# Optimization experiments

Hardware: AMD Instinct MI355X
Metric: run time of the kernel (lower is better)

## Reference

```python
import jax, jax.numpy as jnp
from jax import lax
import numpy as np

B, S = 128, 512
TARGET_SIZE = 32
T = TARGET_SIZE + 4  # tag_size, START = T-2, END = T-1


def setup_inputs() -> dict:
    key = jax.random.key(0)
    k1, k2, k3, k4 = jax.random.split(key, 4)
    feats = jax.random.normal(k1, (B, S, T), dtype=jnp.float32)
    # contiguous-prefix mask (lengths in [S//2, S])
    lengths = jax.random.randint(k2, (B,), S // 2, S + 1)
    mask = (jnp.arange(S)[None, :] < lengths[:, None]).astype(jnp.int32)
    tags = jax.random.randint(k3, (B, S), 0, TARGET_SIZE).astype(jnp.int32)
    # learned transitions, with the hard constraints from __init__
    transitions = 0.1 * jax.random.normal(k4, (T, T), dtype=jnp.float32)
    transitions = transitions.at[:, T - 2].set(-1000.0)  # nothing -> START
    transitions = transitions.at[T - 1, :].set(-1000.0)  # END -> nothing
    return {"feats": feats, "transitions": transitions, "mask": mask, "tags": tags}


def _nll(feats, transitions, mask, tags):
    # feats: (B,S,T), transitions: (T,T) with [i,j] = score(prev=i -> cur=j)
    b, s, t = feats.shape
    START, END = t - 2, t - 1
    fdtype = feats.dtype

    feats_t = jnp.swapaxes(feats, 0, 1)   # (S,B,T)
    mask_t = jnp.swapaxes(mask, 0, 1)     # (S,B)

    # ---- forward algorithm (partition function) ----
    # scores[t,b,i,j] = feats[b,t,j] + transitions[i,j]
    part0 = feats_t[0] + transitions[START][None, :]  # (B,T): alpha after step 0

    def step(part, xs):
        f_step, m_step = xs  # (B,T), (B,)
        # cur[b,i,j] = feats[b,j] + trans[i,j] + part[b,i]
        cur = f_step[:, None, :] + transitions[None, :, :] + part[:, :, None]
        new_part = jax.nn.logsumexp(cur, axis=1)  # (B,T)
        part = jnp.where(m_step[:, None].astype(bool), new_part, part)
        return part, None

    part, _ = lax.scan(step, part0, (feats_t[1:], mask_t[1:]))
    final = jax.nn.logsumexp(part[:, :, None] + transitions[None, :, :], axis=1)  # (B,T)
    forward_score = jnp.sum(final[:, END])

    # ---- gold score ----
    tags_i = tags.astype(jnp.int32)
    prev_tags = jnp.concatenate(
        [jnp.full((b, 1), START, dtype=jnp.int32), tags_i[:, :-1]], axis=1)  # (B,S)
    emit = jnp.take_along_axis(feats, tags_i[:, :, None], axis=2)[:, :, 0]    # (B,S)
    trans_sc = transitions[prev_tags, tags_i]                                  # (B,S)
    tg_energy = jnp.sum((emit + trans_sc) * mask.astype(fdtype))
    lengths = jnp.sum(mask, axis=1).astype(jnp.int32)                          # (B,)
    end_ids = jnp.take_along_axis(tags_i, (lengths - 1)[:, None], axis=1)[:, 0]
    end_energy = jnp.sum(transitions[end_ids, END])
    gold_score = tg_energy + end_energy

    # average_batch = True
    return (forward_score - gold_score) / jnp.asarray(b, fdtype)


def reference(feats, transitions, mask, tags):
    return _nll(feats, transitions, mask, tags)
```

## Files before the change

kernel.cpp:

```cpp
#include <hip/hip_runtime.h>
#include <hip/hip_bf16.h>


namespace {
constexpr int kB = 128;
constexpr int kS = 512;
constexpr int kT = 36;
constexpr int kStart = 34;
constexpr int kEnd = 35;
constexpr int kP = 16;
constexpr int kL = 32;
constexpr int kEStr = 48;

typedef __bf16 bf16x4 __attribute__((ext_vector_type(4)));
typedef short short4 __attribute__((ext_vector_type(4)));
typedef float f32x4 __attribute__((ext_vector_type(4)));

__device__ __forceinline__ float readlane_f(float v, int lane) {
    return __builtin_bit_cast(float, __builtin_amdgcn_readlane(__builtin_bit_cast(int, v), lane));
}

__device__ __forceinline__ float wave_sum(float v) {
#pragma unroll
    for (int off = 32; off; off >>= 1) v += __shfl_xor(v, off, 64);
    return v;
}

__device__ __forceinline__ int wave_sum_i(int v) {
#pragma unroll
    for (int off = 32; off; off >>= 1) v += __shfl_xor(v, off, 64);
    return v;
}

#define MF16(a, b, c) __builtin_amdgcn_mfma_f32_16x16x16bf16_1k((a), (b), (c), 0, 0, 0)


__global__ __attribute__((amdgpu_flat_work_group_size(64, 64),
                          amdgpu_waves_per_eu(2, 4)))
void crf_chunk_kernel(const float* __restrict__ feats,
                      const float* __restrict__ trans,
                      const int* __restrict__ mask,
                      __bf16* __restrict__ Hws,
                      float* __restrict__ lscws) {
    const int b = blockIdx.x;
    const int p = blockIdx.y;
    const int tid = threadIdx.x;
    const int ln = tid & 15;
    const int quad = tid >> 4;

    __shared__ __align__(16) float Etab[kL * kEStr];

    const int* mb = mask + b * kS;
    int len = 0;
    for (int k = tid; k < kS; k += 64) len += mb[k];
    len = wave_sum_i(len);

    __bf16* Hout = Hws + (size_t)(b * kP + p) * (kT * kT);
    const int cs = (p == 0) ? 1 : p * kL;
    const int ce = min((p + 1) * kL, len);
    const int nsteps = ce - cs;

    if (nsteps <= 0) {
        for (int idx = tid; idx < kT * kT; idx += 64)
            Hout[idx] = (__bf16)((idx / kT == idx % kT) ? 1.f : 0.f);
        if (tid == 0) lscws[b * kP + p] = 0.f;
        return;
    }

    const float* fb = feats + ((size_t)b * kS + cs) * kT;
    for (int idx = tid; idx < kL * kEStr; idx += 64) {
        const int tl = idx / kEStr, jj = idx % kEStr;
        Etab[idx] = (jj < kT) ? __expf(fb[tl * kT + jj]) : 1.0f;
    }
    __builtin_amdgcn_s_waitcnt(0);

    auto afrag = [&](int rt, int kc) {
        bf16x4 r;
        const int m = rt * 16 + ln;
#pragma unroll
        for (int e = 0; e < 4; ++e) {
            const int k = kc * 16 + quad * 4 + e;
            float v = 0.f;
            if (m < kT && k < kT) v = __expf(trans[k * kT + m]);
            r[e] = (__bf16)v;
        }
        return __builtin_bit_cast(short4, r);
    };
    const short4 a00 = afrag(0, 0), a01 = afrag(0, 1), a02 = afrag(0, 2);
    const short4 a10 = afrag(1, 0), a11 = afrag(1, 1), a12 = afrag(1, 2);
    const short4 a20 = afrag(2, 0), a21 = afrag(2, 1), a22 = afrag(2, 2);

    auto binit = [&](int kc, int ct) {
        bf16x4 r;
        const int n = ct * 16 + ln;
#pragma unroll
        for (int e = 0; e < 4; ++e) {
            const int k = kc * 16 + quad * 4 + e;
            r[e] = (__bf16)((k == n && k < kT) ? 1.f : 0.f);
        }
        return __builtin_bit_cast(short4, r);
    };
    short4 b00 = binit(0, 0), b01 = binit(0, 1), b02 = binit(0, 2);
    short4 b10 = binit(1, 0), b11 = binit(1, 1), b12 = binit(1, 2);
    short4 b20 = binit(2, 0), b21 = binit(2, 1), b22 = binit(2, 2);

    float logC = 0.f;
    const f32x4 z = {0.f, 0.f, 0.f, 0.f};
    for (int tl = 0; tl < nsteps; ++tl) {
        const f32x4 e0 = *(const f32x4*)&Etab[tl * kEStr + 0 + quad * 4];
        const f32x4 e1 = *(const f32x4*)&Etab[tl * kEStr + 16 + quad * 4];
        const f32x4 e2 = *(const f32x4*)&Etab[tl * kEStr + 32 + quad * 4];

        f32x4 c00 = MF16(a00, b00, z); f32x4 c01 = MF16(a00, b01, z); f32x4 c02 = MF16(a00, b02, z);
        c00 = MF16(a01, b10, c00);     c01 = MF16(a01, b11, c01);     c02 = MF16(a01, b12, c02);
        c00 = MF16(a02, b20, c00);     c01 = MF16(a02, b21, c01);     c02 = MF16(a02, b22, c02);
        f32x4 c10 = MF16(a10, b00, z); f32x4 c11 = MF16(a10, b01, z); f32x4 c12 = MF16(a10, b02, z);
        c10 = MF16(a11, b10, c10);     c11 = MF16(a11, b11, c11);     c12 = MF16(a11, b12, c12);
        c10 = MF16(a12, b20, c10);     c11 = MF16(a12, b21, c11);     c12 = MF16(a12, b22, c12);
        f32x4 c20 = MF16(a20, b00, z); f32x4 c21 = MF16(a20, b01, z); f32x4 c22 = MF16(a20, b02, z);
        c20 = MF16(a21, b10, c20);     c21 = MF16(a21, b11, c21);     c22 = MF16(a21, b12, c22);
        c20 = MF16(a22, b20, c20);     c21 = MF16(a22, b21, c21);     c22 = MF16(a22, b22, c22);

        float rs = 1.f;
        if ((tl & 3) == 3) {
            const float s = readlane_f(c00[1], 1);
            rs = __builtin_amdgcn_rcpf(s);
            logC += __logf(s);
        }
        const f32x4 s0 = e0 * rs, s1 = e1 * rs, s2 = e2 * rs;

#define PK(cv, sv) ({ const f32x4 t_ = (cv) * (sv); bf16x4 h_;                  \
        h_[0] = (__bf16)t_[0]; h_[1] = (__bf16)t_[1];                           \
        h_[2] = (__bf16)t_[2]; h_[3] = (__bf16)t_[3];                           \
        __builtin_bit_cast(short4, h_); })
        b00 = PK(c00, s0); b01 = PK(c01, s0); b02 = PK(c02, s0);
        b10 = PK(c10, s1); b11 = PK(c11, s1); b12 = PK(c12, s1);
        b20 = PK(c20, s2); b21 = PK(c21, s2); b22 = PK(c22, s2);
#undef PK
    }

#define STOREB(Bv, kc, ct) {                                                    \
    const bf16x4 h_ = __builtin_bit_cast(bf16x4, Bv);                           \
    const int n_ = (ct)*16 + ln;                                                \
    _Pragma("unroll") for (int e = 0; e < 4; ++e) {                             \
        const int m_ = (kc)*16 + quad * 4 + e;                                  \
        if (m_ < kT && n_ < kT) Hout[m_ * kT + n_] = h_[e]; } }
    STOREB(b00, 0, 0) STOREB(b01, 0, 1) STOREB(b02, 0, 2)
    STOREB(b10, 1, 0) STOREB(b11, 1, 1) STOREB(b12, 1, 2)
    STOREB(b20, 2, 0) STOREB(b21, 2, 1) STOREB(b22, 2, 2)
#undef STOREB
    if (tid == 0) lscws[b * kP + p] = logC;
}


#define FORK36(X) \
    X(0,0,0,0) X(1,1,0,1) X(2,2,0,2) X(3,3,0,3) \
    X(4,0,1,0) X(5,1,1,1) X(6,2,1,2) X(7,3,1,3) \
    X(8,0,2,0) X(9,1,2,1) X(10,2,2,2) X(11,3,2,3) \
    X(12,0,3,0) X(13,1,3,1) X(14,2,3,2) X(15,3,3,3) \
    X(16,0,4,0) X(17,1,4,1) X(18,2,4,2) X(19,3,4,3) \
    X(20,0,5,0) X(21,1,5,1) X(22,2,5,2) X(23,3,5,3) \
    X(24,0,6,0) X(25,1,6,1) X(26,2,6,2) X(27,3,6,3) \
    X(28,0,7,0) X(29,1,7,1) X(30,2,7,2) X(31,3,7,3) \
    X(32,0,8,0) X(33,1,8,1) X(34,2,8,2) X(35,3,8,3)

__global__ __attribute__((amdgpu_flat_work_group_size(64, 64),
                          amdgpu_waves_per_eu(1, 1)))
void crf_combine_kernel(const float* __restrict__ feats,
                        const float* __restrict__ trans,
                        const int* __restrict__ mask,
                        const int* __restrict__ tags,
                        const __bf16* __restrict__ Hws,
                        const float* __restrict__ lscws,
                        float* __restrict__ out) {
    const int b = blockIdx.x;
    const int j = threadIdx.x;
    const float* fbase = feats + (size_t)b * kS * kT;
    const int* mb = mask + b * kS;
    const int* tb = tags + b * kS;

    int len = 0;
    for (int k = j; k < kS; k += 64) len += mb[k];
    len = wave_sum_i(len);

    const float ME = (j < kT) ? __expf(trans[j * kT + kEnd]) : 0.f;

    float a0 = -1e30f;
    if (j < kT) a0 = fbase[j] + trans[kStart * kT + j];
    float C = readlane_f(a0, 0);
    float q = __expf(a0 - C);

    const int jr = (j < kT) ? j : 0;
#pragma unroll
    for (int p = 0; p < kP; ++p) {
        const __bf16* rp = Hws + ((size_t)(b * kP + p) * kT + jr) * kT;
        const bf16x4 h0 = *(const bf16x4*)(rp + 0);
        const bf16x4 h1 = *(const bf16x4*)(rp + 4);
        const bf16x4 h2 = *(const bf16x4*)(rp + 8);
        const bf16x4 h3 = *(const bf16x4*)(rp + 12);
        const bf16x4 h4 = *(const bf16x4*)(rp + 16);
        const bf16x4 h5 = *(const bf16x4*)(rp + 20);
        const bf16x4 h6 = *(const bf16x4*)(rp + 24);
        const bf16x4 h7 = *(const bf16x4*)(rp + 28);
        const bf16x4 h8 = *(const bf16x4*)(rp + 32);
#define BRD2(n, a, g, c) const float bb##n = readlane_f(q, n);
        FORK36(BRD2)
#undef BRD2
        float v0 = 0.f, v1 = 0.f, v2 = 0.f, v3 = 0.f;
#define FMA2(n, a, g, c) v##a = fmaf(bb##n, (float)h##g[c], v##a);
        FORK36(FMA2)
#undef FMA2
        const float qn = (v0 + v1) + (v2 + v3);
        q = (j < kT) ? qn : 0.f;
        C += lscws[b * kP + p];
        const float s = readlane_f(q, 0);
        q *= __builtin_amdgcn_rcpf(s);
        C += __logf(s);
    }

    const float ssum = wave_sum(q * ME);
    const float forward_b = C + __logf(ssum);

    float g = 0.f;
    for (int k = j; k < kS; k += 64) {
        if (k < len) {
            const int tg = tb[k];
            const int pv = (k == 0) ? kStart : tb[k - 1];
            g += fbase[(size_t)k * kT + tg] + trans[pv * kT + tg];
        }
    }
    g = wave_sum(g);

    if (j == 0) {
        g += trans[tb[len - 1] * kT + kEnd];
        atomicAdd(out, (forward_b - g) * (1.0f / kB));
    }
}

}

extern "C" void kernel_launch(void* const* d_in, const int* in_sizes, int n_in,
                              void* d_out, int out_size, void* d_ws, size_t ws_size,
                              hipStream_t stream) {
    const float* feats = (const float*)d_in[0];
    const float* trans = (const float*)d_in[1];
    const int* mask = (const int*)d_in[2];
    const int* tags = (const int*)d_in[3];
    float* out = (float*)d_out;

    __bf16* Hws = (__bf16*)d_ws;
    float* lscws = (float*)(Hws + (size_t)kB * kP * kT * kT);

    (void)hipMemsetAsync(out, 0, sizeof(float), stream);
    crf_chunk_kernel<<<dim3(kB, kP), dim3(64), 0, stream>>>(feats, trans, mask, Hws, lscws);
    crf_combine_kernel<<<dim3(kB), dim3(64), 0, stream>>>(feats, trans, mask, tags,
                                                          Hws, lscws, out);
}
```

Before: 111.4 us.

## Halve chunk length to double chunk parallelism and read rescale from bf16 state

Splits the sequence into 32 chunks of 16 steps instead of 16 chunks of 32, so each chunk kernel has a shorter serial matrix-product chain and twice as many blocks run in parallel. The combine kernel then processes twice as many chunk matrices, and its loop is only partially unrolled. The rescale factor is now read from the packed bf16 state before the MFMAs, which takes the readlane off the critical path. Feature staging and the mask sum are unrolled to batch global loads before the exp writes to LDS.

```diff
diff --git a/kernel.cpp b/kernel.cpp
--- a/kernel.cpp
+++ b/kernel.cpp
@@ -8,13 +8,14 @@
 constexpr int kT = 36;
 constexpr int kStart = 34;
 constexpr int kEnd = 35;
-constexpr int kP = 16;
-constexpr int kL = 32;
-constexpr int kEStr = 48;
+constexpr int kP = 32;
+constexpr int kL = 16;
+constexpr int kEStr = 64;
 
 typedef __bf16 bf16x4 __attribute__((ext_vector_type(4)));
-typedef short short4 __attribute__((ext_vector_type(4)));
+typedef short short4v __attribute__((ext_vector_type(4)));
 typedef float f32x4 __attribute__((ext_vector_type(4)));
+typedef int int2v __attribute__((ext_vector_type(2)));
 
 __device__ __forceinline__ float readlane_f(float v, int lane) {
     return __builtin_bit_cast(float, __builtin_amdgcn_readlane(__builtin_bit_cast(int, v), lane));
@@ -52,7 +53,8 @@
 
     const int* mb = mask + b * kS;
     int len = 0;
-    for (int k = tid; k < kS; k += 64) len += mb[k];
+#pragma unroll
+    for (int k = 0; k < kS / 64; ++k) len += mb[k * 64 + tid];
     len = wave_sum_i(len);
 
     __bf16* Hout = Hws + (size_t)(b * kP + p) * (kT * kT);
@@ -68,9 +70,14 @@
     }
 
     const float* fb = feats + ((size_t)b * kS + cs) * kT;
-    for (int idx = tid; idx < kL * kEStr; idx += 64) {
-        const int tl = idx / kEStr, jj = idx % kEStr;
-        Etab[idx] = (jj < kT) ? __expf(fb[tl * kT + jj]) : 1.0f;
+    {
+        float stage[kL];
+#pragma unroll
+        for (int it = 0; it < kL; ++it)
+            stage[it] = (tid < kT) ? fb[it * kT + tid] : 0.f;
+#pragma unroll
+        for (int it = 0; it < kL; ++it)
+            Etab[it * kEStr + tid] = (tid < kT) ? __expf(stage[it]) : 1.0f;
     }
     __builtin_amdgcn_s_waitcnt(0);
 
@@ -84,11 +91,11 @@
             if (m < kT && k < kT) v = __expf(trans[k * kT + m]);
             r[e] = (__bf16)v;
         }
-        return __builtin_bit_cast(short4, r);
+        return __builtin_bit_cast(short4v, r);
     };
-    const short4 a00 = afrag(0, 0), a01 = afrag(0, 1), a02 = afrag(0, 2);
-    const short4 a10 = afrag(1, 0), a11 = afrag(1, 1), a12 = afrag(1, 2);
-    const short4 a20 = afrag(2, 0), a21 = afrag(2, 1), a22 = afrag(2, 2);
+    const short4v a00 = afrag(0, 0), a01 = afrag(0, 1), a02 = afrag(0, 2);
+    const short4v a10 = afrag(1, 0), a11 = afrag(1, 1), a12 = afrag(1, 2);
+    const short4v a20 = afrag(2, 0), a21 = afrag(2, 1), a22 = afrag(2, 2);
 
     auto binit = [&](int kc, int ct) {
         bf16x4 r;
@@ -98,18 +105,20 @@
             const int k = kc * 16 + quad * 4 + e;
             r[e] = (__bf16)((k == n && k < kT) ? 1.f : 0.f);
         }
-        return __builtin_bit_cast(short4, r);
+        return __builtin_bit_cast(short4v, r);
     };
-    short4 b00 = binit(0, 0), b01 = binit(0, 1), b02 = binit(0, 2);
-    short4 b10 = binit(1, 0), b11 = binit(1, 1), b12 = binit(1, 2);
-    short4 b20 = binit(2, 0), b21 = binit(2, 1), b22 = binit(2, 2);
+    short4v b00 = binit(0, 0), b01 = binit(0, 1), b02 = binit(0, 2);
+    short4v b10 = binit(1, 0), b11 = binit(1, 1), b12 = binit(1, 2);
+    short4v b20 = binit(2, 0), b21 = binit(2, 1), b22 = binit(2, 2);
 
     float logC = 0.f;
     const f32x4 z = {0.f, 0.f, 0.f, 0.f};
     for (int tl = 0; tl < nsteps; ++tl) {
-        const f32x4 e0 = *(const f32x4*)&Etab[tl * kEStr + 0 + quad * 4];
-        const f32x4 e1 = *(const f32x4*)&Etab[tl * kEStr + 16 + quad * 4];
-        const f32x4 e2 = *(const f32x4*)&Etab[tl * kEStr + 32 + quad * 4];
+        const int w11 = __builtin_amdgcn_readlane(__builtin_bit_cast(int2v, b00).x, 1);
+        const float* et = &Etab[tl * kEStr + quad * 4];
+        const f32x4 e0 = *(const f32x4*)(et + 0);
+        const f32x4 e1 = *(const f32x4*)(et + 16);
+        const f32x4 e2 = *(const f32x4*)(et + 32);
 
         f32x4 c00 = MF16(a00, b00, z); f32x4 c01 = MF16(a00, b01, z); f32x4 c02 = MF16(a00, b02, z);
         c00 = MF16(a01, b10, c00);     c01 = MF16(a01, b11, c01);     c02 = MF16(a01, b12, c02);
@@ -123,7 +132,7 @@
 
         float rs = 1.f;
         if ((tl & 3) == 3) {
-            const float s = readlane_f(c00[1], 1);
+            const float s = __builtin_bit_cast(float, (unsigned)w11 & 0xFFFF0000u);
             rs = __builtin_amdgcn_rcpf(s);
             logC += __logf(s);
         }
@@ -132,7 +141,7 @@
 #define PK(cv, sv) ({ const f32x4 t_ = (cv) * (sv); bf16x4 h_;                  \
         h_[0] = (__bf16)t_[0]; h_[1] = (__bf16)t_[1];                           \
         h_[2] = (__bf16)t_[2]; h_[3] = (__bf16)t_[3];                           \
-        __builtin_bit_cast(short4, h_); })
+        __builtin_bit_cast(short4v, h_); })
         b00 = PK(c00, s0); b01 = PK(c01, s0); b02 = PK(c02, s0);
         b10 = PK(c10, s1); b11 = PK(c11, s1); b12 = PK(c12, s1);
         b20 = PK(c20, s2); b21 = PK(c21, s2); b22 = PK(c22, s2);
@@ -180,7 +189,8 @@
     const int* tb = tags + b * kS;
 
     int len = 0;
-    for (int k = j; k < kS; k += 64) len += mb[k];
+#pragma unroll
+    for (int k = 0; k < kS / 64; ++k) len += mb[k * 64 + j];
     len = wave_sum_i(len);
 
     const float ME = (j < kT) ? __expf(trans[j * kT + kEnd]) : 0.f;
@@ -191,7 +201,7 @@
     float q = __expf(a0 - C);
 
     const int jr = (j < kT) ? j : 0;
-#pragma unroll
+#pragma unroll 4
     for (int p = 0; p < kP; ++p) {
         const __bf16* rp = Hws + ((size_t)(b * kP + p) * kT + jr) * kT;
         const bf16x4 h0 = *(const bf16x4*)(rp + 0);
```

New measurement: 109.6 us. No clear change (-1.7%).
